# Kernel tuning notes

Measured on AMD Instinct MI355X. Metric: run time of the kernel, lower is better.

## Reference

```python
import jax, jax.numpy as jnp
import numpy as np

# --- static config (mirrors args) ---
FOV = 79.0
RES = 5                      # map_resolution (cm/cell)
MAP_SIZE_CM = 4800           # map_size_cm // global_downscaling
VR = 100                     # vision_range (cells)
CAM_H_CM = 88.0              # camera_height * 100
CAT_THR, EXP_THR, MAP_THR = 5.0, 1.0, 1.0
MAX_H = 72                   # int(360 / 5)
MIN_H = -8                   # int(-40 / 5)
DEG = 57.29577951308232


def _splat(feat, coords, dims):
    """Trilinear splat (scatter-add) of feat [F,N] at coords [3,N] in [-1,1] into grid dims, then round."""
    F_, N = feat.shape
    Mtot = dims[0] * dims[1] * dims[2]
    pos = [coords[d] * dims[d] / 2.0 + dims[d] / 2.0 for d in range(3)]
    flo = [jnp.floor(p) for p in pos]
    grid = jnp.zeros((F_, Mtot), jnp.float32)
    for c0 in (0, 1):
        for c1 in (0, 1):
            for c2 in (0, 1):
                idx = jnp.zeros((N,), jnp.float32)
                wts = jnp.ones((N,), jnp.float32)
                for d, off in enumerate((c0, c1, c2)):
                    p = flo[d] + off
                    safe = ((p > 0) & (p < dims[d])).astype(jnp.float32)
                    wts = wts * (1.0 - jnp.abs(pos[d] - p)) * safe
                    idx = idx * dims[d] + p * safe
                grid = grid.at[:, idx.astype(jnp.int32)].add(feat * wts[None, :])
    return jnp.round(grid).reshape(F_, dims[0], dims[1], dims[2])


def _affine_grid(theta, H, W):
    # align_corners=True base grid; theta [2,3] -> grid [H,W,2] (x,y)
    gx, gy = jnp.meshgrid(jnp.linspace(-1.0, 1.0, W), jnp.linspace(-1.0, 1.0, H))
    base = jnp.stack([gx, gy, jnp.ones_like(gx)], -1)  # [H,W,3]
    return base @ theta.T


def _grid_sample(img, grid):
    # bilinear, zero padding, align_corners=True. img [C,H,W], grid [H,W,2]
    C, H, W = img.shape
    x = (grid[..., 0] + 1.0) * 0.5 * (W - 1)
    y = (grid[..., 1] + 1.0) * 0.5 * (H - 1)
    x0 = jnp.floor(x); y0 = jnp.floor(y)
    out = jnp.zeros_like(img)
    for yy, xx in ((y0, x0), (y0, x0 + 1), (y0 + 1, x0), (y0 + 1, x0 + 1)):
        w = (1.0 - jnp.abs(x - xx)) * (1.0 - jnp.abs(y - yy))
        inb = ((xx >= 0) & (xx <= W - 1) & (yy >= 0) & (yy <= H - 1)).astype(img.dtype)
        xi = jnp.clip(xx, 0, W - 1).astype(jnp.int32)
        yi = jnp.clip(yy, 0, H - 1).astype(jnp.int32)
        out = out + img[:, yi, xi] * (w * inb)[None]
    return out


def _forward(obs, pose_obs, maps_last, poses_last):
    bs, c, h, w = obs.shape
    depth = obs[0, 3]  # [h,w] in cm
    # camera matrix
    xc = (w - 1.0) / 2.0
    zc = (h - 1.0) / 2.0
    f = (w / 2.0) / np.tan(np.deg2rad(FOV / 2.0))
    gx = jnp.arange(w, dtype=jnp.float32)[None, :]
    gz = jnp.arange(h - 1, -1, -1, dtype=jnp.float32)[:, None]
    X = (gx - xc) * depth / f
    Z = (gz - zc) * depth / f
    # camera->agent (elevation 0 -> identity rot) then shift_loc (theta=pi/2 -> identity rot)
    X = X + VR * RES // 2
    Z = Z + CAM_H_CM
    zdim = MAX_H - MIN_H
    xs = (X / RES - VR // 2.0) / VR * 2.0
    ys = (depth / RES - VR // 2.0) / VR * 2.0
    zs = (Z / RES - (MAX_H + MIN_H) // 2.0) / zdim * 2.0
    N = h * w
    coords = jnp.stack([xs.reshape(N), ys.reshape(N), zs.reshape(N)], 0)  # [3,N]
    feat = jnp.concatenate([jnp.ones((1, N), jnp.float32), obs[0, 4:].reshape(c - 4, N)], 0)  # [F,N]
    voxels = _splat(feat, coords, (VR, VR, zdim))       # [F,VR,VR,Z]
    voxels = jnp.swapaxes(voxels, 1, 2)                  # .transpose(2,3)
    min_z = int(25 / RES - MIN_H)                        # 13
    max_z = int((CAM_H_CM + 1) / RES - MIN_H)            # 25
    ahp = voxels[..., min_z:max_z].sum(-1)               # [F,VR,VR]
    allp = voxels.sum(-1)
    fp_map = jnp.clip(ahp[0:1] / MAP_THR, 0.0, 1.0)
    fp_exp = jnp.clip(allp[0:1] / EXP_THR, 0.0, 1.0)
    M = MAP_SIZE_CM // RES
    x1 = M // 2 - VR // 2; x2 = x1 + VR
    y1 = M // 2; y2 = y1 + VR
    agent_view = jnp.zeros((c, M, M), jnp.float32)
    agent_view = agent_view.at[0:1, y1:y2, x1:x2].set(fp_map)
    agent_view = agent_view.at[1:2, y1:y2, x1:x2].set(fp_exp)
    agent_view = agent_view.at[4:, y1:y2, x1:x2].set(jnp.clip(ahp[1:] / CAT_THR, 0.0, 1.0))
    # pose integration (note: pose_pred aliases poses_last which is updated in-place in torch)
    th = poses_last[2] / DEG
    ny = poses_last[1] + pose_obs[0] * jnp.sin(th) + pose_obs[1] * jnp.cos(th)
    nx = poses_last[0] + pose_obs[0] * jnp.cos(th) - pose_obs[1] * jnp.sin(th)
    nt = poses_last[2] + pose_obs[2] * DEG
    nt = jnp.fmod(nt - 180.0, 360.0) + 180.0
    nt = jnp.fmod(nt + 180.0, 360.0) - 180.0
    current_pose = jnp.stack([nx, ny, nt])
    # spatial transform (st_pose is detached in torch)
    st = jax.lax.stop_gradient(current_pose)
    half = M // 2
    sx = -(st[0] * 100.0 / RES - half) / half
    sy = -(st[1] * 100.0 / RES - half) / half
    sth = (90.0 - st[2]) * np.pi / 180.0
    ct, sn = jnp.cos(sth), jnp.sin(sth)
    z = jnp.zeros(()); o = jnp.ones(())
    theta1 = jnp.stack([jnp.stack([ct, -sn, z]), jnp.stack([sn, ct, z])])
    theta2 = jnp.stack([jnp.stack([o, z, sx]), jnp.stack([z, o, sy])])
    rotated = _grid_sample(agent_view, _affine_grid(theta1, M, M))
    translated = _grid_sample(rotated, _affine_grid(theta2, M, M))
    # snap positive semantic cells (channels 4..7) to per-channel feature max
    ks = feat[1:5].max(axis=1)  # [4]
    sem = translated[4:8]
    translated = translated.at[4:8].set(jnp.where(sem > 0.0, ks[:, None, None], sem))
    map_pred = jnp.maximum(maps_last, translated)
    return fp_map, map_pred, current_pose, current_pose


def setup_inputs() -> dict:
    key = jax.random.key(0)
    k1, k2, k3, k4 = jax.random.split(key, 4)
    C = 9
    obs = jax.random.uniform(k1, (1, C, 480, 640), dtype=jnp.float32)
    obs = obs.at[:, 3].set(obs[:, 3] * 400.0 + 50.0)  # depth in cm, 50..450
    pose_obs = jax.random.uniform(k2, (3,), dtype=jnp.float32) * jnp.array([0.2, 0.2, 0.1], jnp.float32)
    maps_last = jax.random.uniform(k3, (C, 960, 960), dtype=jnp.float32)
    poses_last = jnp.array([24.0, 24.0, 0.0], jnp.float32) + jax.random.uniform(k4, (3,), dtype=jnp.float32) * jnp.array([2.0, 2.0, 30.0], jnp.float32)
    return {"obs": obs, "pose_obs": pose_obs, "maps_last": maps_last, "poses_last": poses_last}


def reference(obs, pose_obs, maps_last, poses_last):
    return _forward(obs, pose_obs, maps_last, poses_last)
```

## Files before the change

kernel.cpp:

```cpp
#include <hip/hip_runtime.h>
#include <math.h>

#define NPIX (480*640)
#define MDIM 960
#define MPIX (MDIM*MDIM)
#define PACK_M 307201u
#define CNT_STRIDE 32

#define SCAL_OFF 0
#define OFFS_OFF 80
#define SM_OFF   10084
#define PACK_OFF 80084
#define POS_OFF  387284
#define FEAT_OFF 1616084

#define OUT_FPMAP 0
#define OUT_MAP   10000
#define OUT_POSE  (10000 + 9*MPIX)

__global__ __launch_bounds__(256) void count_kernel(const float* __restrict__ obs,
                                                    unsigned* __restrict__ cnt,
                                                    unsigned* __restrict__ pack,
                                                    float fcam) {
    int p = blockIdx.x*256 + threadIdx.x;
    int i = p / 640, j = p - i*640;
    float d = obs[3*NPIX + p];
    float X = ((float)j - 319.5f) * d / fcam + 250.0f;
    float Z = ((float)(479 - i) - 239.5f) * d / fcam + 88.0f;
    float xs = ((X/5.0f - 50.0f)/100.0f)*2.0f;
    float ys = ((d/5.0f - 50.0f)/100.0f)*2.0f;
    float zs = ((Z/5.0f - 32.0f)/80.0f)*2.0f;
    float pos0 = (xs*100.0f)/2.0f + 50.0f;
    float pos1 = (ys*100.0f)/2.0f + 50.0f;
    float pos2 = (zs*80.0f)/2.0f + 40.0f;
    int bx = (int)floorf(pos0), by = (int)floorf(pos1), bz = (int)floorf(pos2);
    unsigned pk = 0xFFFFFFFFu;
    if (bx >= 0 && bx <= 99 && by >= 0 && by <= 99 && bz >= 0 && bz <= 79) {
        unsigned b = (unsigned)(bx*100 + by);
        unsigned rank = atomicAdd(&cnt[b*CNT_STRIDE], 1u);
        pk = b * PACK_M + rank;
    }
    pack[p] = pk;
}

__global__ __launch_bounds__(256) void scan_pose_kernel(const unsigned* __restrict__ cnt,
                                                        unsigned* __restrict__ offs,
                                                        const float* pose_obs,
                                                        const float* poses_last,
                                                        float* scal, float* out_pose) {
    int tid = threadIdx.x;
    int lane = tid & 63, wave = tid >> 6;
    if (tid < 4) scal[16*(tid+1)] = 0.0f;
    unsigned lc[40];
    unsigned sum = 0;
    #pragma unroll
    for (int q = 0; q < 40; q++) {
        int idx = tid*40 + q;
        lc[q] = (idx < 10000) ? cnt[idx*CNT_STRIDE] : 0u;
        sum += lc[q];
    }
    unsigned incl = sum;
    #pragma unroll
    for (int off = 1; off < 64; off <<= 1) {
        unsigned u = (unsigned)__shfl_up((int)incl, off, 64);
        if (lane >= off) incl += u;
    }
    __shared__ unsigned wtot[4];
    if (lane == 63) wtot[wave] = incl;
    __syncthreads();
    unsigned pre = 0;
    for (int w = 0; w < wave; w++) pre += wtot[w];
    unsigned excl = pre + incl - sum;
    unsigned run = excl;
    #pragma unroll
    for (int q = 0; q < 40; q++) {
        int idx = tid*40 + q;
        if (idx < 10000) { offs[idx] = run; run += lc[q]; }
    }
    if (tid == 255) {
        offs[10000] = excl;
        const float DEGc = 57.29577951308232f;
        float th = poses_last[2] / DEGc;
        float s = sinf(th), c = cosf(th);
        float ny = poses_last[1] + pose_obs[0]*s + pose_obs[1]*c;
        float nx = poses_last[0] + pose_obs[0]*c - pose_obs[1]*s;
        float nt = poses_last[2] + pose_obs[2]*DEGc;
        nt = fmodf(nt - 180.0f, 360.0f) + 180.0f;
        nt = fmodf(nt + 180.0f, 360.0f) - 180.0f;
        out_pose[0] = nx; out_pose[1] = ny; out_pose[2] = nt;
        out_pose[3] = nx; out_pose[4] = ny; out_pose[5] = nt;
        float sx = -((nx*100.0f)/5.0f - 480.0f)/480.0f;
        float sy = -((ny*100.0f)/5.0f - 480.0f)/480.0f;
        float sth = ((90.0f - nt) * 3.14159265358979323846f) / 180.0f;
        scal[0] = cosf(sth);
        scal[1] = sinf(sth);
        scal[2] = sx;
        scal[3] = sy;
    }
}

__global__ __launch_bounds__(256) void scatter_kernel(const float* __restrict__ obs,
                                                      const unsigned* __restrict__ offs,
                                                      const unsigned* __restrict__ pack,
                                                      float4* __restrict__ pos,
                                                      float4* __restrict__ feat,
                                                      float* scal, float fcam) {
    int p = blockIdx.x*256 + threadIdx.x;
    int i = p / 640, j = p - i*640;
    unsigned pk = pack[p];
    float d  = obs[3*NPIX + p];
    float f1 = obs[4*NPIX + p];
    float f2 = obs[5*NPIX + p];
    float f3 = obs[6*NPIX + p];
    float f4 = obs[7*NPIX + p];
    float f5 = obs[8*NPIX + p];
    if (pk != 0xFFFFFFFFu) {
        unsigned b = pk / PACK_M;
        unsigned rank = pk - b * PACK_M;
        unsigned k = offs[b] + rank;
        float X = ((float)j - 319.5f) * d / fcam + 250.0f;
        float Z = ((float)(479 - i) - 239.5f) * d / fcam + 88.0f;
        float xs = ((X/5.0f - 50.0f)/100.0f)*2.0f;
        float ys = ((d/5.0f - 50.0f)/100.0f)*2.0f;
        float zs = ((Z/5.0f - 32.0f)/80.0f)*2.0f;
        float pos0 = (xs*100.0f)/2.0f + 50.0f;
        float pos1 = (ys*100.0f)/2.0f + 50.0f;
        float pos2 = (zs*80.0f)/2.0f + 40.0f;
        pos[k]  = make_float4(pos0, pos1, pos2, f1);
        feat[k] = make_float4(f2, f3, f4, f5);
    }
    float m0 = f1, m1 = f2, m2 = f3, m3 = f4;
    #pragma unroll
    for (int off = 32; off > 0; off >>= 1) {
        m0 = fmaxf(m0, __shfl_down(m0, off, 64));
        m1 = fmaxf(m1, __shfl_down(m1, off, 64));
        m2 = fmaxf(m2, __shfl_down(m2, off, 64));
        m3 = fmaxf(m3, __shfl_down(m3, off, 64));
    }
    __shared__ float red[4][4];
    int lane = threadIdx.x & 63, wave = threadIdx.x >> 6;
    if (lane == 0) {
        red[wave][0] = m0; red[wave][1] = m1; red[wave][2] = m2; red[wave][3] = m3;
    }
    __syncthreads();
    if (threadIdx.x < 4) {
        int c = threadIdx.x;
        float m = fmaxf(fmaxf(red[0][c], red[1][c]), fmaxf(red[2][c], red[3][c]));
        atomicMax((int*)&scal[16*(c+1)], __float_as_int(m));
    }
}

__global__ __launch_bounds__(256) void gather_kernel(const float4* __restrict__ pos,
                                                     const float4* __restrict__ feat,
                                                     const unsigned* __restrict__ offs,
                                                     float* __restrict__ sm,
                                                     float* __restrict__ out_fp) {
    int wave = threadIdx.x >> 6, lane = threadIdx.x & 63;
    int y  = blockIdx.x / 25;
    int gi = blockIdx.x % 25;
    int xg = (gi == 0) ? 12 : ((gi & 1) ? (12 + (gi+1)/2) : (12 - gi/2));
    int x = xg*4 + wave;
    __shared__ float slabs[4][488];
    float* za = slabs[wave];
    for (int q = lane; q < 480; q += 64) za[q] = 0.0f;
    __syncthreads();
    if (x >= 1 && y >= 1) {
        int b0 = (x-1)*100 + (y-1);
        int b1 = x*100 + (y-1);
        unsigned s0 = offs[b0], e0 = offs[b0+2];
        unsigned s1 = offs[b1], e1 = offs[b1+2];
        unsigned n0 = e0 - s0, n = n0 + (e1 - s1);
        float xf = (float)x, yf = (float)y;
        for (unsigned idx = lane; idx < n; idx += 64) {
            unsigned k = (idx < n0) ? (s0 + idx) : (s1 + idx - n0);
            float4 a = pos[k];
            float w0 = 1.0f - fabsf(a.x - xf);
            float w1 = 1.0f - fabsf(a.y - yf);
            float w01 = w0 * w1;
            float bzf = floorf(a.z);
            bool need = (bzf >= 12.0f) && (bzf < 25.0f);
            float4 q2 = need ? feat[k] : make_float4(0.f, 0.f, 0.f, 0.f);
            #pragma unroll
            for (int c2 = 0; c2 <= 1; c2++) {
                float p2 = bzf + (float)c2;
                if (!(p2 > 0.0f && p2 < 80.0f)) continue;
                float w = w01 * (1.0f - fabsf(a.z - p2));
                int zi = (int)p2;
                int zb = zi * 6;
                atomicAdd(&za[zb + 0], w);
                if (zi >= 13 && zi < 25) {
                    atomicAdd(&za[zb + 1], w*a.w);
                    atomicAdd(&za[zb + 2], w*q2.x);
                    atomicAdd(&za[zb + 3], w*q2.y);
                    atomicAdd(&za[zb + 4], w*q2.z);
                    atomicAdd(&za[zb + 5], w*q2.w);
                }
            }
        }
    }
    __syncthreads();
    int z = lane;
    float r0 = rintf(za[z*6 + 0]);
    float all0 = r0;
    if (lane < 16) all0 += rintf(za[(z + 64)*6 + 0]);
    bool inb = (z >= 13 && z < 25);
    float a0 = inb ? r0 : 0.0f;
    float a1 = inb ? rintf(za[z*6 + 1]) : 0.0f;
    float a2 = inb ? rintf(za[z*6 + 2]) : 0.0f;
    float a3 = inb ? rintf(za[z*6 + 3]) : 0.0f;
    float a4 = inb ? rintf(za[z*6 + 4]) : 0.0f;
    float a5 = inb ? rintf(za[z*6 + 5]) : 0.0f;
    #pragma unroll
    for (int off = 32; off > 0; off >>= 1) {
        all0 += __shfl_down(all0, off, 64);
        a0 += __shfl_down(a0, off, 64);
        a1 += __shfl_down(a1, off, 64);
        a2 += __shfl_down(a2, off, 64);
        a3 += __shfl_down(a3, off, 64);
        a4 += __shfl_down(a4, off, 64);
        a5 += __shfl_down(a5, off, 64);
    }
    if (lane == 0) {
        int t = y*100 + x;
        float fp = fminf(a0, 1.0f);
        float ex = fminf(all0, 1.0f);
        sm[0*10000 + t] = fp;
        sm[1*10000 + t] = ex;
        sm[2*10000 + t] = fminf(a1/5.0f, 1.0f);
        sm[3*10000 + t] = fminf(a2/5.0f, 1.0f);
        sm[4*10000 + t] = fminf(a3/5.0f, 1.0f);
        sm[5*10000 + t] = fminf(a4/5.0f, 1.0f);
        sm[6*10000 + t] = fminf(a5/5.0f, 1.0f);
        out_fp[t] = fp;
    }
}

__device__ __forceinline__ void sample_agent(float gxv, float gyv,
                                             float ct, float sn,
                                             const float* __restrict__ sm,
                                             float rot[7]) {
    float u = ct*gxv - sn*gyv;
    float v = sn*gxv + ct*gyv;
    float xim = ((u + 1.0f)*0.5f)*959.0f;
    float yim = ((v + 1.0f)*0.5f)*959.0f;
    float x0 = floorf(xim), y0 = floorf(yim);
    #pragma unroll
    for (int ty = 0; ty <= 1; ty++) {
        float yy = y0 + (float)ty;
        if (yy < 480.0f || yy >= 580.0f) continue;
        float wy = 1.0f - fabsf(yim - yy);
        int yi = (int)yy - 480;
        #pragma unroll
        for (int tx = 0; tx <= 1; tx++) {
            float xx = x0 + (float)tx;
            if (xx < 430.0f || xx >= 530.0f) continue;
            float w = (1.0f - fabsf(xim - xx)) * wy;
            int o = yi*100 + ((int)xx - 430);
            #pragma unroll
            for (int k = 0; k < 7; k++) rot[k] += sm[k*10000 + o] * w;
        }
    }
}

__device__ __forceinline__ void pixel_ts(float xim, float yim, float ct, float sn,
                                         const float* __restrict__ sm, float ts[7]) {
    const float step = 2.0f/959.0f;
    float x0 = floorf(xim), y0 = floorf(yim);
    #pragma unroll
    for (int ty = 0; ty <= 1; ty++) {
        float yy = y0 + (float)ty;
        if (yy < 0.0f || yy > 959.0f) continue;
        float wy = 1.0f - fabsf(yim - yy);
        #pragma unroll
        for (int tx = 0; tx <= 1; tx++) {
            float xx = x0 + (float)tx;
            if (xx < 0.0f || xx > 959.0f) continue;
            float w = (1.0f - fabsf(xim - xx)) * wy;
            float rot[7] = {0,0,0,0,0,0,0};
            float gx1 = xx*step - 1.0f;
            float gy1 = yy*step - 1.0f;
            sample_agent(gx1, gy1, ct, sn, sm, rot);
            #pragma unroll
            for (int k = 0; k < 7; k++) ts[k] += rot[k]*w;
        }
    }
}

__global__ __launch_bounds__(256) void final_kernel(const float* __restrict__ maps_last,
                                                    const float* __restrict__ sm,
                                                    const float* __restrict__ scal,
                                                    float* __restrict__ out_map) {
    int g = blockIdx.x*256 + threadIdx.x;
    int p = g*4;
    int y = p / MDIM, xp = p - y*MDIM;
    float ct = scal[0], sn = scal[1], sx = scal[2], sy = scal[3];
    const float step = 2.0f/959.0f;
    float gyv = (float)y*step - 1.0f;
    float v = gyv + sy;
    float yim = ((v + 1.0f)*0.5f)*959.0f;
    float gyc = yim*step - 1.0f;
    float xims[4];
    bool act[4];
    bool any = false;
    #pragma unroll
    for (int q = 0; q < 4; q++) {
        float gxv = (float)(xp+q)*step - 1.0f;
        float u = gxv + sx;
        float xim = ((u + 1.0f)*0.5f)*959.0f;
        xims[q] = xim;
        float gxc = xim*step - 1.0f;
        float uc = ct*gxc - sn*gyc;
        float vc = sn*gxc + ct*gyc;
        float xc2 = ((uc + 1.0f)*0.5f)*959.0f;
        float yc2 = ((vc + 1.0f)*0.5f)*959.0f;
        bool a = (xc2 > 427.5f) && (xc2 < 531.5f) && (yc2 > 477.5f) && (yc2 < 581.5f);
        act[q] = a;
        any = any || a;
    }
    if (!any) {
        #pragma unroll
        for (int c = 0; c < 9; c++) {
            float4 ml = *(const float4*)(maps_last + c*MPIX + p);
            float4 o;
            o.x = fmaxf(ml.x, 0.0f); o.y = fmaxf(ml.y, 0.0f);
            o.z = fmaxf(ml.z, 0.0f); o.w = fmaxf(ml.w, 0.0f);
            *(float4*)(out_map + c*MPIX + p) = o;
        }
        return;
    }
    float ks0 = scal[16], ks1 = scal[32], ks2 = scal[48], ks3 = scal[64];
    #pragma unroll
    for (int q = 0; q < 4; q++) {
        int o = p + q;
        float ts[7] = {0,0,0,0,0,0,0};
        if (act[q]) pixel_ts(xims[q], yim, ct, sn, sm, ts);
        float ml;
        ml = maps_last[0*MPIX + o]; out_map[0*MPIX + o] = fmaxf(ml, ts[0]);
        ml = maps_last[1*MPIX + o]; out_map[1*MPIX + o] = fmaxf(ml, ts[1]);
        ml = maps_last[2*MPIX + o]; out_map[2*MPIX + o] = fmaxf(ml, 0.0f);
        ml = maps_last[3*MPIX + o]; out_map[3*MPIX + o] = fmaxf(ml, 0.0f);
        float t4 = ts[2]; t4 = (t4 > 0.0f) ? ks0 : t4;
        ml = maps_last[4*MPIX + o]; out_map[4*MPIX + o] = fmaxf(ml, t4);
        float t5 = ts[3]; t5 = (t5 > 0.0f) ? ks1 : t5;
        ml = maps_last[5*MPIX + o]; out_map[5*MPIX + o] = fmaxf(ml, t5);
        float t6 = ts[4]; t6 = (t6 > 0.0f) ? ks2 : t6;
        ml = maps_last[6*MPIX + o]; out_map[6*MPIX + o] = fmaxf(ml, t6);
        float t7 = ts[5]; t7 = (t7 > 0.0f) ? ks3 : t7;
        ml = maps_last[7*MPIX + o]; out_map[7*MPIX + o] = fmaxf(ml, t7);
        ml = maps_last[8*MPIX + o]; out_map[8*MPIX + o] = fmaxf(ml, ts[6]);
    }
}

extern "C" void kernel_launch(void* const* d_in, const int* in_sizes, int n_in,
                              void* d_out, int out_size, void* d_ws, size_t ws_size,
                              hipStream_t stream) {
    const float* obs        = (const float*)d_in[0];
    const float* pose_obs   = (const float*)d_in[1];
    const float* maps_last  = (const float*)d_in[2];
    const float* poses_last = (const float*)d_in[3];
    float* out = (float*)d_out;

    unsigned* ws_u = (unsigned*)d_ws;
    float*    ws_f = (float*)d_ws;
    float*    scal = ws_f + SCAL_OFF;
    unsigned* offs = ws_u + OFFS_OFF;
    float*    sm   = ws_f + SM_OFF;
    unsigned* pack = ws_u + PACK_OFF;
    float4*   pos  = (float4*)(ws_f + POS_OFF);
    float4*   feat = (float4*)(ws_f + FEAT_OFF);
    unsigned* cnt  = ws_u + POS_OFF;

    hipMemsetAsync(ws_f + POS_OFF, 0, (size_t)10000 * CNT_STRIDE * 4u, stream);

    float fcam = (float)(320.0 / tan(39.5 * M_PI / 180.0));

    count_kernel<<<1200, 256, 0, stream>>>(obs, cnt, pack, fcam);
    scan_pose_kernel<<<1, 256, 0, stream>>>(cnt, offs, pose_obs, poses_last,
                                            scal, out + OUT_POSE);
    scatter_kernel<<<1200, 256, 0, stream>>>(obs, offs, pack, pos, feat, scal, fcam);
    gather_kernel<<<2500, 256, 0, stream>>>(pos, feat, offs, sm, out + OUT_FPMAP);
    final_kernel<<<900, 256, 0, stream>>>(maps_last, sm, scal, out + OUT_MAP);
}
```

Before: 248.8 us.

## Give each gather cell a full block and use nontemporal loads/stores in final copy

The gather kernel now assigns one 256-thread block per map cell instead of one wave per cell. All four waves split that cell's points and accumulate into private shared-memory slabs, which are then summed before wave 0 does the reduction. The feature load is made unconditional. The fast path of the final kernel switches to nontemporal vector loads and stores for the maps_last copy to avoid cache pollution. This spreads load-imbalanced dense cells across more threads, at the cost of 4x more blocks and extra syncs, mostly idle for sparse cells.

```diff
diff --git a/kernel.cpp b/kernel.cpp
--- a/kernel.cpp
+++ b/kernel.cpp
@@ -17,6 +17,14 @@
 #define OUT_FPMAP 0
 #define OUT_MAP   10000
 #define OUT_POSE  (10000 + 9*MPIX)
+
+typedef float __attribute__((ext_vector_type(4))) f32x4;
+__device__ __forceinline__ f32x4 ntload4(const float* p) {
+    return __builtin_nontemporal_load((const f32x4*)p);
+}
+__device__ __forceinline__ void ntstore4(float* p, f32x4 v) {
+    __builtin_nontemporal_store(v, (f32x4*)p);
+}
 
 __global__ __launch_bounds__(256) void count_kernel(const float* __restrict__ obs,
                                                     unsigned* __restrict__ cnt,
@@ -156,10 +164,7 @@
                                                      float* __restrict__ sm,
                                                      float* __restrict__ out_fp) {
     int wave = threadIdx.x >> 6, lane = threadIdx.x & 63;
-    int y  = blockIdx.x / 25;
-    int gi = blockIdx.x % 25;
-    int xg = (gi == 0) ? 12 : ((gi & 1) ? (12 + (gi+1)/2) : (12 - gi/2));
-    int x = xg*4 + wave;
+    int x = blockIdx.x % 100, y = blockIdx.x / 100;
     __shared__ float slabs[4][488];
     float* za = slabs[wave];
     for (int q = lane; q < 480; q += 64) za[q] = 0.0f;
@@ -171,15 +176,14 @@
         unsigned s1 = offs[b1], e1 = offs[b1+2];
         unsigned n0 = e0 - s0, n = n0 + (e1 - s1);
         float xf = (float)x, yf = (float)y;
-        for (unsigned idx = lane; idx < n; idx += 64) {
+        for (unsigned idx = threadIdx.x; idx < n; idx += 256) {
             unsigned k = (idx < n0) ? (s0 + idx) : (s1 + idx - n0);
-            float4 a = pos[k];
+            float4 a  = pos[k];
+            float4 q2 = feat[k];
             float w0 = 1.0f - fabsf(a.x - xf);
             float w1 = 1.0f - fabsf(a.y - yf);
             float w01 = w0 * w1;
             float bzf = floorf(a.z);
-            bool need = (bzf >= 12.0f) && (bzf < 25.0f);
-            float4 q2 = need ? feat[k] : make_float4(0.f, 0.f, 0.f, 0.f);
             #pragma unroll
             for (int c2 = 0; c2 <= 1; c2++) {
                 float p2 = bzf + (float)c2;
@@ -199,39 +203,45 @@
         }
     }
     __syncthreads();
-    int z = lane;
-    float r0 = rintf(za[z*6 + 0]);
-    float all0 = r0;
-    if (lane < 16) all0 += rintf(za[(z + 64)*6 + 0]);
-    bool inb = (z >= 13 && z < 25);
-    float a0 = inb ? r0 : 0.0f;
-    float a1 = inb ? rintf(za[z*6 + 1]) : 0.0f;
-    float a2 = inb ? rintf(za[z*6 + 2]) : 0.0f;
-    float a3 = inb ? rintf(za[z*6 + 3]) : 0.0f;
-    float a4 = inb ? rintf(za[z*6 + 4]) : 0.0f;
-    float a5 = inb ? rintf(za[z*6 + 5]) : 0.0f;
-    #pragma unroll
-    for (int off = 32; off > 0; off >>= 1) {
-        all0 += __shfl_down(all0, off, 64);
-        a0 += __shfl_down(a0, off, 64);
-        a1 += __shfl_down(a1, off, 64);
-        a2 += __shfl_down(a2, off, 64);
-        a3 += __shfl_down(a3, off, 64);
-        a4 += __shfl_down(a4, off, 64);
-        a5 += __shfl_down(a5, off, 64);
-    }
-    if (lane == 0) {
-        int t = y*100 + x;
-        float fp = fminf(a0, 1.0f);
-        float ex = fminf(all0, 1.0f);
-        sm[0*10000 + t] = fp;
-        sm[1*10000 + t] = ex;
-        sm[2*10000 + t] = fminf(a1/5.0f, 1.0f);
-        sm[3*10000 + t] = fminf(a2/5.0f, 1.0f);
-        sm[4*10000 + t] = fminf(a3/5.0f, 1.0f);
-        sm[5*10000 + t] = fminf(a4/5.0f, 1.0f);
-        sm[6*10000 + t] = fminf(a5/5.0f, 1.0f);
-        out_fp[t] = fp;
+    for (int q = threadIdx.x; q < 480; q += 256) {
+        slabs[0][q] = slabs[0][q] + slabs[1][q] + slabs[2][q] + slabs[3][q];
+    }
+    __syncthreads();
+    if (wave == 0) {
+        int z = lane;
+        float r0 = rintf(slabs[0][z*6 + 0]);
+        float all0 = r0;
+        if (lane < 16) all0 += rintf(slabs[0][(z + 64)*6 + 0]);
+        bool inb = (z >= 13 && z < 25);
+        float a0 = inb ? r0 : 0.0f;
+        float a1 = inb ? rintf(slabs[0][z*6 + 1]) : 0.0f;
+        float a2 = inb ? rintf(slabs[0][z*6 + 2]) : 0.0f;
+        float a3 = inb ? rintf(slabs[0][z*6 + 3]) : 0.0f;
+        float a4 = inb ? rintf(slabs[0][z*6 + 4]) : 0.0f;
+        float a5 = inb ? rintf(slabs[0][z*6 + 5]) : 0.0f;
+        #pragma unroll
+        for (int off = 32; off > 0; off >>= 1) {
+            all0 += __shfl_down(all0, off, 64);
+            a0 += __shfl_down(a0, off, 64);
+            a1 += __shfl_down(a1, off, 64);
+            a2 += __shfl_down(a2, off, 64);
+            a3 += __shfl_down(a3, off, 64);
+            a4 += __shfl_down(a4, off, 64);
+            a5 += __shfl_down(a5, off, 64);
+        }
+        if (lane == 0) {
+            int t = y*100 + x;
+            float fp = fminf(a0, 1.0f);
+            float ex = fminf(all0, 1.0f);
+            sm[0*10000 + t] = fp;
+            sm[1*10000 + t] = ex;
+            sm[2*10000 + t] = fminf(a1/5.0f, 1.0f);
+            sm[3*10000 + t] = fminf(a2/5.0f, 1.0f);
+            sm[4*10000 + t] = fminf(a3/5.0f, 1.0f);
+            sm[5*10000 + t] = fminf(a4/5.0f, 1.0f);
+            sm[6*10000 + t] = fminf(a5/5.0f, 1.0f);
+            out_fp[t] = fp;
+        }
     }
 }
 
@@ -320,11 +330,11 @@
     if (!any) {
         #pragma unroll
         for (int c = 0; c < 9; c++) {
-            float4 ml = *(const float4*)(maps_last + c*MPIX + p);
-            float4 o;
+            f32x4 ml = ntload4(maps_last + c*MPIX + p);
+            f32x4 o;
             o.x = fmaxf(ml.x, 0.0f); o.y = fmaxf(ml.y, 0.0f);
             o.z = fmaxf(ml.z, 0.0f); o.w = fmaxf(ml.w, 0.0f);
-            *(float4*)(out_map + c*MPIX + p) = o;
+            ntstore4(out_map + c*MPIX + p, o);
         }
         return;
     }
@@ -378,6 +388,6 @@
     scan_pose_kernel<<<1, 256, 0, stream>>>(cnt, offs, pose_obs, poses_last,
                                             scal, out + OUT_POSE);
     scatter_kernel<<<1200, 256, 0, stream>>>(obs, offs, pack, pos, feat, scal, fcam);
-    gather_kernel<<<2500, 256, 0, stream>>>(pos, feat, offs, sm, out + OUT_FPMAP);
+    gather_kernel<<<10000, 256, 0, stream>>>(pos, feat, offs, sm, out + OUT_FPMAP);
     final_kernel<<<900, 256, 0, stream>>>(maps_last, sm, scal, out + OUT_MAP);
 }
```

Result: faster. 223.1 us (-10.3%).
